# Kernel tuning notes

Measured on AMD Instinct MI355X. Metric: run time of the kernel, lower is better.

## Reference

```python
import jax, jax.numpy as jnp
import numpy as np

B, S, D, E, K = 4, 2048, 1024, 8, 2
H = 4 * D  # SwiGLU hidden size


def setup_inputs() -> dict:
    key = jax.random.key(0)
    ks = jax.random.split(key, 6)
    s = 0.02
    return {
        "x": jax.random.normal(ks[0], (B, S, D), dtype=jnp.float32),
        "Wr": jax.random.normal(ks[1], (D, E), dtype=jnp.float32) * s,
        "br": jnp.zeros((E,), jnp.float32),
        "Wg": jax.random.normal(ks[2], (E, D, H), dtype=jnp.float32) * s,
        "bg": jnp.zeros((E, H), jnp.float32),
        "Wu": jax.random.normal(ks[3], (E, D, H), dtype=jnp.float32) * s,
        "bu": jnp.zeros((E, H), jnp.float32),
        "Wd": jax.random.normal(ks[4], (E, H, D), dtype=jnp.float32) * s,
        "bd": jnp.zeros((E, D), jnp.float32),
        "top_k": K,
    }


def reference(x, Wr, br, Wg, bg, Wu, bu, Wd, bd, top_k):
    # Router: top-k over expert logits, softmax over the selected k values.
    Bx, Sx, Dx = x.shape
    Ex = Wr.shape[-1]
    logits = x @ Wr + br                              # [B,S,E]
    vals, idx = jax.lax.top_k(logits, top_k)          # [B,S,K]
    probs = jax.nn.softmax(vals, axis=-1)             # [B,S,K]
    # Dense per-token expert weight; 0 for experts the token is not routed to.
    gate_w = jnp.sum(jax.nn.one_hot(idx, Ex, dtype=x.dtype) * probs[..., None], axis=-2)  # [B,S,E]

    xt = x.reshape(-1, Dx)          # [T,D]
    gw = gate_w.reshape(-1, Ex).T   # [E,T]

    def body(acc, p):
        wg, bgi, wu, bui, wd, bdi, ge = p
        h = jax.nn.silu(xt @ wg + bgi) * (xt @ wu + bui)   # [T,4D]
        y = (h @ wd + bdi) * ge[:, None]                   # zero where ge==0 (not routed)
        return acc + y, None

    out, _ = jax.lax.scan(body, jnp.zeros_like(xt), (Wg, bg, Wu, bu, Wd, bd, gw))
    return out.reshape(Bx, Sx, Dx)
```

## Files before the change

kernel.cpp:

```cpp
#include <hip/hip_runtime.h>
#include <hip/hip_fp16.h>


#define T_TOK 8192
#define D_IN  1024
#define E_EXP 8
#define H_HID 4096
#define NSLOT (T_TOK * 2)
#define NSLOT_PAD (NSLOT + 256)
#define KSPLIT 4

typedef _Float16 f16;
typedef __attribute__((ext_vector_type(8))) _Float16 f16x8;
typedef __attribute__((ext_vector_type(4))) _Float16 f16x4;
typedef __attribute__((ext_vector_type(4))) float f32x4;

__device__ __forceinline__ void gload_lds16(const void* g, void* l) {
  __builtin_amdgcn_global_load_lds(
      (const __attribute__((address_space(1))) unsigned int*)g,
      (__attribute__((address_space(3))) unsigned int*)l, 16, 0, 0);
}


__global__ __launch_bounds__(256) void prep_kernel(
    const float* __restrict__ x, const float* __restrict__ Wr,
    const float* __restrict__ br, const float* __restrict__ Wg,
    const float* __restrict__ Wu, const float* __restrict__ Wd,
    int* __restrict__ eidx, float2* __restrict__ pval,
    int* __restrict__ counts, f16* __restrict__ xb,
    f16* __restrict__ wgut, f16* __restrict__ wdt) {
  __shared__ float tile[128][33];
  int g = blockIdx.x;
  if (g < T_TOK / 4) {
    int lane = threadIdx.x & 63, wid = threadIdx.x >> 6;
    int t = g * 4 + wid;
    const float* xr = x + (size_t)t * D_IN;
    float s[8] = {0.f, 0.f, 0.f, 0.f, 0.f, 0.f, 0.f, 0.f};
    int dbase = lane * 16;
#pragma unroll
    for (int i = 0; i < 4; ++i) {
      float4 xv = *(const float4*)(xr + dbase + i * 4);
      f16x4 xo = {(f16)xv.x, (f16)xv.y, (f16)xv.z, (f16)xv.w};
      *(f16x4*)(xb + (size_t)t * D_IN + dbase + i * 4) = xo;
      const float xs[4] = {xv.x, xv.y, xv.z, xv.w};
#pragma unroll
      for (int j = 0; j < 4; ++j) {
        const float* wr = Wr + (size_t)(dbase + i * 4 + j) * E_EXP;
        float4 w0 = *(const float4*)wr;
        float4 w1 = *(const float4*)(wr + 4);
        float xvj = xs[j];
        s[0] += xvj * w0.x; s[1] += xvj * w0.y; s[2] += xvj * w0.z; s[3] += xvj * w0.w;
        s[4] += xvj * w1.x; s[5] += xvj * w1.y; s[6] += xvj * w1.z; s[7] += xvj * w1.w;
      }
    }
#pragma unroll
    for (int off = 32; off; off >>= 1)
#pragma unroll
      for (int e = 0; e < 8; ++e) s[e] += __shfl_xor(s[e], off);
    if (lane == 0) {
      float v[8];
#pragma unroll
      for (int e = 0; e < 8; ++e) v[e] = s[e] + br[e];
      int i0 = 0; float v0 = v[0];
#pragma unroll
      for (int e = 1; e < 8; ++e) if (v[e] > v0) { v0 = v[e]; i0 = e; }
      int i1 = -1; float v1 = -1e30f;
#pragma unroll
      for (int e = 0; e < 8; ++e)
        if (e != i0 && v[e] > v1) { v1 = v[e]; i1 = e; }
      float ed = __expf(v1 - v0);
      float inv = 1.f / (1.f + ed);
      eidx[t] = i0 | (i1 << 8);
      pval[t] = make_float2(inv, ed * inv);
      atomicAdd(&counts[i0], 1);
      atomicAdd(&counts[i1], 1);
    }
    return;
  }
  int i = g - T_TOK / 4;
  int which = i >> 13;
  int j = i & 8191;
  const float* src; f16* dst; int R, C, MAP, cx, cy, e; size_t dstride;
  if (which < 2) {
    cx = j & 127; cy = (j >> 7) & 7; e = j >> 10;
    R = D_IN; C = H_HID; dstride = (size_t)2 * H_HID * D_IN;
    dst = wgut; src = (which == 0) ? Wg : Wu; MAP = which + 1;
  } else {
    cx = j & 31; cy = (j >> 5) & 31; e = j >> 10;
    R = H_HID; C = D_IN; dstride = (size_t)D_IN * H_HID;
    dst = wdt; src = Wd; MAP = 0;
  }
  const float* s = src + (size_t)e * R * C;
  f16* d = dst + (size_t)e * dstride;
  int c0 = cx * 32, r0 = cy * 128;
#pragma unroll
  for (int q4 = 0; q4 < 4; ++q4) {
    int q = q4 * 256 + threadIdx.x;
    int r = q >> 3, c4 = (q & 7) * 4;
    float4 v = *(const float4*)(s + (size_t)(r0 + r) * C + c0 + c4);
    tile[r][c4 + 0] = v.x; tile[r][c4 + 1] = v.y;
    tile[r][c4 + 2] = v.z; tile[r][c4 + 3] = v.w;
  }
  __syncthreads();
#pragma unroll
  for (int w2 = 0; w2 < 2; ++w2) {
    int w = w2 * 256 + threadIdx.x;
    int col = w >> 4, oct = w & 15;
    int c = c0 + col;
    int ro = (MAP == 0) ? c : (((c >> 4) << 5) + ((MAP == 2) ? 16 : 0) + (c & 15));
    f16x8 o;
#pragma unroll
    for (int k = 0; k < 8; ++k) o[k] = (f16)tile[oct * 8 + k][col];
    *(f16x8*)(d + (size_t)ro * R + r0 + oct * 8) = o;
  }
}

__global__ void scan_kernel(const int* __restrict__ counts, int* __restrict__ offsets) {
  if (threadIdx.x == 0) {
    int acc = 0;
#pragma unroll
    for (int e = 0; e < E_EXP; ++e) { offsets[e] = acc; acc += counts[e]; }
    offsets[E_EXP] = acc;
  }
}

__global__ __launch_bounds__(256) void scatter_kernel(
    const int* __restrict__ eidx, const float2* __restrict__ pval,
    const int* __restrict__ offsets, int* __restrict__ cursors,
    int* __restrict__ perm, float* __restrict__ gatew, int2* __restrict__ slotAB) {
  int t = blockIdx.x * 256 + threadIdx.x;
  if (t >= T_TOK) return;
  int ei = eidx[t];
  float2 p = pval[t];
  int e0 = ei & 0xff, e1 = (ei >> 8) & 0xff;
  int s0 = offsets[e0] + atomicAdd(&cursors[e0], 1);
  perm[s0] = t; gatew[s0] = p.x;
  int s1 = offsets[e1] + atomicAdd(&cursors[e1], 1);
  perm[s1] = t; gatew[s1] = p.y;
  slotAB[t] = make_int2(s0, s1);
}


#define BAR __builtin_amdgcn_s_barrier()
#define VMCNT(N) asm volatile("s_waitcnt vmcnt(" #N ")" ::: "memory")

#define STAGE_(B, ISB, H, KT, BASE) do {                                   \
  char* d_ = smem + (B)*32768 + (ISB)*16384 + (H)*8192 + wid*1024;         \
  gload_lds16(BASE[(H)*2+0] + (size_t)(KT)*64, d_);                        \
  gload_lds16(BASE[(H)*2+1] + (size_t)(KT)*64, d_ + 4096);                 \
} while (0)

#define LDA_(B, Q)                                                          \
  _Pragma("unroll")                                                         \
  for (int m_ = 0; m_ < 2; ++m_) {                                          \
    fa[m_][0] = *(const f16x8*)(smem + (B)*32768 + aoff + ((Q)*2+m_)*2048 + offk0); \
    fa[m_][1] = *(const f16x8*)(smem + (B)*32768 + aoff + ((Q)*2+m_)*2048 + offk1); \
  }

#define LDB_(FB, B, RH)                                                     \
  _Pragma("unroll")                                                         \
  for (int n_ = 0; n_ < 2; ++n_) {                                          \
    FB[n_][0] = *(const f16x8*)(smem + (B)*32768 + 16384 + boff + ((RH)*2+n_)*2048 + offk0); \
    FB[n_][1] = *(const f16x8*)(smem + (B)*32768 + 16384 + boff + ((RH)*2+n_)*2048 + offk1); \
  }

#define QUAD_(Q, RH, FB)                                                    \
  __builtin_amdgcn_s_setprio(1);                                            \
  _Pragma("unroll")                                                         \
  for (int m_ = 0; m_ < 2; ++m_)                                            \
    _Pragma("unroll")                                                       \
    for (int n_ = 0; n_ < 2; ++n_) {                                        \
      acc[(Q)*2+m_][(RH)*2+n_] = __builtin_amdgcn_mfma_f32_16x16x32_f16(    \
          fa[m_][0], FB[n_][0], acc[(Q)*2+m_][(RH)*2+n_], 0, 0, 0);         \
      acc[(Q)*2+m_][(RH)*2+n_] = __builtin_amdgcn_mfma_f32_16x16x32_f16(    \
          fa[m_][1], FB[n_][1], acc[(Q)*2+m_][(RH)*2+n_], 0, 0, 0);         \
    }                                                                       \
  __builtin_amdgcn_s_setprio(0);

template<int MODE>
__global__ __launch_bounds__(256, 2) void ffn_8ph_kernel(
    const f16* __restrict__ Asrc, const f16* __restrict__ Bsrc,
    const float* __restrict__ bias0, const float* __restrict__ bias1,
    const int* __restrict__ offsets, const int* __restrict__ perm,
    const float* __restrict__ gatew, f16* __restrict__ dst) {
  constexpr int KD = MODE ? H_HID : D_IN;
  constexpr int BROWS = MODE ? D_IN : 2 * H_HID;
  constexpr int NT = 16;

  __shared__ __align__(16) char smem[65536];

  int g = blockIdx.x;
  int xcd = g & 7;
  int e, nt, kc, mt;
  if constexpr (MODE == 0) {
    mt = (g >> 3) & 63;
    int panel = xcd + 8 * (g >> 9);
    e = panel >> 6; nt = panel & 63; kc = 0;
  } else {
    int j = g >> 3;
    nt = j & 7;
    mt = (j >> 3) & 63;
    int group = xcd + 8 * (j >> 9);
    e = group >> 2; kc = group & 3;
  }

  int off = offsets[e];
  int cnt = offsets[e + 1] - off;
  if (mt * 128 >= cnt) return;

  int tid = threadIdx.x, lane = tid & 63, wid = tid >> 6;
  int wm = wid >> 1, wn = wid & 1;
  int l15 = lane & 15, lc0 = lane >> 4, s7 = l15 & 7;
  int aoff = (wm * 64 + l15) * 128;
  int boff = (wn * 64 + l15) * 128;
  int offk0 = ((lc0) ^ s7) * 16;
  int offk1 = ((lc0 + 4) ^ s7) * 16;

  int rowh_[2], lc_[2];
#pragma unroll
  for (int i = 0; i < 2; ++i) {
    int chunk = i * 256 + tid;
    rowh_[i] = chunk >> 3;
    lc_[i] = (chunk & 7) ^ (rowh_[i] & 7);
  }

  const f16 *aB[4], *bB[4];
#pragma unroll
  for (int h = 0; h < 2; ++h)
#pragma unroll
    for (int i = 0; i < 2; ++i) {
      int absrow = h * 64 + rowh_[i];
      bB[h * 2 + i] = Bsrc + ((size_t)e * BROWS + nt * 128 + absrow) * KD +
                      kc * 1024 + lc_[i] * 8;
      int slot = off + min(mt * 128 + absrow, cnt - 1);
      if constexpr (MODE == 0)
        aB[h * 2 + i] = Asrc + (size_t)perm[slot] * KD + lc_[i] * 8;
      else
        aB[h * 2 + i] = Asrc + (size_t)slot * KD + kc * 1024 + lc_[i] * 8;
    }

  float bv0[4], bv1[2];
  if constexpr (MODE == 0) {
#pragma unroll
    for (int p = 0; p < 2; ++p) {
      int h = nt * 64 + wn * 32 + p * 16 + l15;
      bv0[p] = bias0[e * H_HID + h];
      bv1[p] = bias1[e * H_HID + h];
    }
  } else {
#pragma unroll
    for (int n = 0; n < 4; ++n)
      bv0[n] = (kc == 0)
                   ? bias0[e * D_IN + nt * 128 + wn * 64 + n * 16 + l15]
                   : 0.f;
  }

  f32x4 acc[4][4] = {};
  f16x8 fa[2][2], fb01[2][2], fb23[2][2];

  STAGE_(0, 1, 0, 0, bB); STAGE_(0, 1, 1, 0, bB);
  STAGE_(0, 0, 0, 0, aB); STAGE_(0, 0, 1, 0, aB);
  STAGE_(1, 1, 0, 1, bB); STAGE_(1, 1, 1, 1, bB);
  STAGE_(1, 0, 0, 1, aB);
  VMCNT(6);
  BAR;

  for (int it = 0; it < NT / 2; ++it) {
    int b_ = 2 * it + 1;
    int a2 = min(2 * it + 2, NT - 1);
    int b2 = min(2 * it + 3, NT - 1);
    LDA_(0, 0); LDB_(fb01, 0, 0); STAGE_(1, 0, 1, b_, aB);
    BAR; QUAD_(0, 0, fb01); BAR;
    LDB_(fb23, 0, 1);
    BAR; QUAD_(0, 1, fb23); BAR;
    LDA_(0, 1); STAGE_(0, 1, 0, a2, bB);
    BAR; QUAD_(1, 0, fb01); BAR;
    STAGE_(0, 1, 1, a2, bB);
    BAR; QUAD_(1, 1, fb23);
    VMCNT(4);
    BAR;
    LDA_(1, 0); LDB_(fb01, 1, 0); STAGE_(0, 0, 0, a2, aB);
    BAR; QUAD_(0, 0, fb01); BAR;
    LDB_(fb23, 1, 1); STAGE_(0, 0, 1, a2, aB);
    BAR; QUAD_(0, 1, fb23); BAR;
    LDA_(1, 1); STAGE_(1, 1, 0, b2, bB);
    BAR; QUAD_(1, 0, fb01); BAR;
    STAGE_(1, 1, 1, b2, bB); STAGE_(1, 0, 0, b2, aB);
    BAR; QUAD_(1, 1, fb23);
    VMCNT(6);
    BAR;
  }

  VMCNT(0);
  __syncthreads();

  int c0_ = lc0 * 4;
  f16* tile = (f16*)smem;
  if constexpr (MODE == 0) {
#pragma unroll
    for (int p = 0; p < 2; ++p) {
      int colL = wn * 32 + p * 16 + l15;
#pragma unroll
      for (int m = 0; m < 4; ++m) {
        int row = wm * 64 + m * 16 + c0_;
#pragma unroll
        for (int r = 0; r < 4; ++r) {
          float gv = acc[m][2 * p][r] + bv0[p];
          float uv = acc[m][2 * p + 1][r] + bv1[p];
          tile[(row + r) * 64 + colL] = (f16)((gv / (1.f + __expf(-gv))) * uv);
        }
      }
    }
    __syncthreads();
    f16* dbase = dst + (size_t)(off + mt * 128) * H_HID + nt * 64;
#pragma unroll
    for (int i = 0; i < 4; ++i) {
      int linear = i * 256 + tid;
      int row = linear >> 3, c8 = linear & 7;
      if (mt * 128 + row < cnt) {
        f16x8 v = *(const f16x8*)&tile[row * 64 + c8 * 8];
        __builtin_nontemporal_store(v, (f16x8*)(dbase + (size_t)row * H_HID + c8 * 8));
      }
    }
  } else {
#pragma unroll
    for (int n = 0; n < 4; ++n) {
      int colL = wn * 64 + n * 16 + l15;
#pragma unroll
      for (int m = 0; m < 4; ++m) {
        int row = wm * 64 + m * 16 + c0_;
#pragma unroll
        for (int r = 0; r < 4; ++r) {
          int slot = off + min(mt * 128 + row + r, cnt - 1);
          tile[(row + r) * 128 + colL] =
              (f16)(gatew[slot] * (acc[m][n][r] + bv0[n]));
        }
      }
    }
    __syncthreads();
    f16* dstP = dst + (size_t)kc * NSLOT_PAD * D_IN;
    f16* dbase = dstP + (size_t)(off + mt * 128) * D_IN + nt * 128;
#pragma unroll
    for (int i = 0; i < 8; ++i) {
      int linear = i * 256 + tid;
      int row = linear >> 4, c16 = linear & 15;
      if (mt * 128 + row < cnt) {
        f16x8 v = *(const f16x8*)&tile[row * 128 + c16 * 8];
        __builtin_nontemporal_store(v, (f16x8*)(dbase + (size_t)row * D_IN + c16 * 8));
      }
    }
  }
}

__global__ __launch_bounds__(256) void combine_kernel(
    const f16* __restrict__ ypart, const int2* __restrict__ slotAB,
    float* __restrict__ out) {
  int i = blockIdx.x * 256 + threadIdx.x;
  int t = i >> 7;
  int c8 = i & 127;
  int2 s = slotAB[t];
  float sum[8] = {0.f, 0.f, 0.f, 0.f, 0.f, 0.f, 0.f, 0.f};
#pragma unroll
  for (int kc = 0; kc < KSPLIT; ++kc) {
    const f16* base = ypart + (size_t)kc * NSLOT_PAD * D_IN + c8 * 8;
    f16x8 y0 = *(const f16x8*)(base + (size_t)s.x * D_IN);
    f16x8 y1 = *(const f16x8*)(base + (size_t)s.y * D_IN);
#pragma unroll
    for (int j = 0; j < 8; ++j) sum[j] += (float)y0[j] + (float)y1[j];
  }
  float* o = out + (size_t)t * D_IN + c8 * 8;
  f32x4 o0 = {sum[0], sum[1], sum[2], sum[3]};
  f32x4 o1 = {sum[4], sum[5], sum[6], sum[7]};
  __builtin_nontemporal_store(o0, (f32x4*)o);
  __builtin_nontemporal_store(o1, (f32x4*)(o + 4));
}


extern "C" void kernel_launch(void* const* d_in, const int* in_sizes, int n_in,
                              void* d_out, int out_size, void* d_ws, size_t ws_size,
                              hipStream_t stream) {
  const float* x  = (const float*)d_in[0];
  const float* Wr = (const float*)d_in[1];
  const float* br = (const float*)d_in[2];
  const float* Wg = (const float*)d_in[3];
  const float* bg = (const float*)d_in[4];
  const float* Wu = (const float*)d_in[5];
  const float* bu = (const float*)d_in[6];
  const float* Wd = (const float*)d_in[7];
  const float* bd = (const float*)d_in[8];
  float* out = (float*)d_out;

  char* ws = (char*)d_ws;
  size_t o = 0;
  auto alloc = [&](size_t bytes) {
    size_t r = o;
    o += (bytes + 255) & ~(size_t)255;
    return r;
  };
  f16* xb     = (f16*)(ws + alloc((size_t)T_TOK * D_IN * 2));
  f16* wgut   = (f16*)(ws + alloc((size_t)E_EXP * 2 * H_HID * D_IN * 2));
  f16* wdt    = (f16*)(ws + alloc((size_t)E_EXP * D_IN * H_HID * 2));
  f16* hbuf   = (f16*)(ws + alloc((size_t)NSLOT_PAD * H_HID * 2));
  int* eidx   = (int*)(ws + alloc((size_t)T_TOK * 4));
  float2* pval= (float2*)(ws + alloc((size_t)T_TOK * 8));
  int* counts = (int*)(ws + alloc(64 * 4));
  int* cursors = counts + 8;
  int* offsets = counts + 16;
  int* perm   = (int*)(ws + alloc((size_t)NSLOT_PAD * 4));
  float* gatew= (float*)(ws + alloc((size_t)NSLOT_PAD * 4));
  int2* slotAB= (int2*)(ws + alloc((size_t)T_TOK * 8));
  f16* ypart  = xb;

  hipMemsetAsync(counts, 0, 64 * 4, stream);

  prep_kernel<<<dim3(T_TOK / 4 + 3 * 8192), 256, 0, stream>>>(
      x, Wr, br, Wg, Wu, Wd, eidx, pval, counts, xb, wgut, wdt);
  scan_kernel<<<1, 64, 0, stream>>>(counts, offsets);
  scatter_kernel<<<T_TOK / 256, 256, 0, stream>>>(eidx, pval, offsets, cursors,
                                                  perm, gatew, slotAB);
  ffn_8ph_kernel<0><<<dim3(32768), 256, 0, stream>>>(
      xb, wgut, bg, bu, offsets, perm, nullptr, hbuf);
  ffn_8ph_kernel<1><<<dim3(16384), 256, 0, stream>>>(
      hbuf, wdt, bd, nullptr, offsets, nullptr, gatew, ypart);
  combine_kernel<<<T_TOK * D_IN / 8 / 256, 256, 0, stream>>>(ypart, slotAB, out);
}
```

Baseline: 906.3 us.

## Remove split-K from down-projection GEMM and simplify combine to two-slot sum

The down-projection kernel no longer splits the 4096-long reduction into four chunks that each write fp16 partial outputs. Each block now runs the full K loop (64 iterations) and writes one output buffer, with the expert taken directly from the XCD index. The combine kernel then reads only two slot rows per token instead of eight. This removes the write and re-read of the extra partial buffers, at the cost of about four times fewer, longer blocks, less parallelism and per-XCD load imbalance when experts receive uneven token counts.

New measurement: 889.2 us. Within noise of the previous version (-1.9%).

```diff
diff --git a/kernel.cpp b/kernel.cpp
--- a/kernel.cpp
+++ b/kernel.cpp
@@ -8,7 +8,6 @@
 #define H_HID 4096
 #define NSLOT (T_TOK * 2)
 #define NSLOT_PAD (NSLOT + 256)
-#define KSPLIT 4
 
 typedef _Float16 f16;
 typedef __attribute__((ext_vector_type(8))) _Float16 f16x8;
@@ -185,23 +184,22 @@
     const float* __restrict__ gatew, f16* __restrict__ dst) {
   constexpr int KD = MODE ? H_HID : D_IN;
   constexpr int BROWS = MODE ? D_IN : 2 * H_HID;
-  constexpr int NT = 16;
+  constexpr int NT = MODE ? 64 : 16;
 
   __shared__ __align__(16) char smem[65536];
 
   int g = blockIdx.x;
   int xcd = g & 7;
-  int e, nt, kc, mt;
+  int e, nt, mt;
   if constexpr (MODE == 0) {
     mt = (g >> 3) & 63;
     int panel = xcd + 8 * (g >> 9);
-    e = panel >> 6; nt = panel & 63; kc = 0;
+    e = panel >> 6; nt = panel & 63;
   } else {
+    e = xcd;
     int j = g >> 3;
     nt = j & 7;
-    mt = (j >> 3) & 63;
-    int group = xcd + 8 * (j >> 9);
-    e = group >> 2; kc = group & 3;
+    mt = j >> 3;
   }
 
   int off = offsets[e];
@@ -231,12 +229,12 @@
     for (int i = 0; i < 2; ++i) {
       int absrow = h * 64 + rowh_[i];
       bB[h * 2 + i] = Bsrc + ((size_t)e * BROWS + nt * 128 + absrow) * KD +
-                      kc * 1024 + lc_[i] * 8;
+                      lc_[i] * 8;
       int slot = off + min(mt * 128 + absrow, cnt - 1);
       if constexpr (MODE == 0)
         aB[h * 2 + i] = Asrc + (size_t)perm[slot] * KD + lc_[i] * 8;
       else
-        aB[h * 2 + i] = Asrc + (size_t)slot * KD + kc * 1024 + lc_[i] * 8;
+        aB[h * 2 + i] = Asrc + (size_t)slot * KD + lc_[i] * 8;
     }
 
   float bv0[4], bv1[2];
@@ -250,9 +248,7 @@
   } else {
 #pragma unroll
     for (int n = 0; n < 4; ++n)
-      bv0[n] = (kc == 0)
-                   ? bias0[e * D_IN + nt * 128 + wn * 64 + n * 16 + l15]
-                   : 0.f;
+      bv0[n] = bias0[e * D_IN + nt * 128 + wn * 64 + n * 16 + l15];
   }
 
   f32x4 acc[4][4] = {};
@@ -338,8 +334,7 @@
       }
     }
     __syncthreads();
-    f16* dstP = dst + (size_t)kc * NSLOT_PAD * D_IN;
-    f16* dbase = dstP + (size_t)(off + mt * 128) * D_IN + nt * 128;
+    f16* dbase = dst + (size_t)(off + mt * 128) * D_IN + nt * 128;
 #pragma unroll
     for (int i = 0; i < 8; ++i) {
       int linear = i * 256 + tid;
@@ -353,24 +348,19 @@
 }
 
 __global__ __launch_bounds__(256) void combine_kernel(
-    const f16* __restrict__ ypart, const int2* __restrict__ slotAB,
+    const f16* __restrict__ ybuf, const int2* __restrict__ slotAB,
     float* __restrict__ out) {
   int i = blockIdx.x * 256 + threadIdx.x;
   int t = i >> 7;
   int c8 = i & 127;
   int2 s = slotAB[t];
-  float sum[8] = {0.f, 0.f, 0.f, 0.f, 0.f, 0.f, 0.f, 0.f};
-#pragma unroll
-  for (int kc = 0; kc < KSPLIT; ++kc) {
-    const f16* base = ypart + (size_t)kc * NSLOT_PAD * D_IN + c8 * 8;
-    f16x8 y0 = *(const f16x8*)(base + (size_t)s.x * D_IN);
-    f16x8 y1 = *(const f16x8*)(base + (size_t)s.y * D_IN);
-#pragma unroll
-    for (int j = 0; j < 8; ++j) sum[j] += (float)y0[j] + (float)y1[j];
-  }
+  f16x8 y0 = *(const f16x8*)(ybuf + (size_t)s.x * D_IN + c8 * 8);
+  f16x8 y1 = *(const f16x8*)(ybuf + (size_t)s.y * D_IN + c8 * 8);
   float* o = out + (size_t)t * D_IN + c8 * 8;
-  f32x4 o0 = {sum[0], sum[1], sum[2], sum[3]};
-  f32x4 o1 = {sum[4], sum[5], sum[6], sum[7]};
+  f32x4 o0 = {(float)y0[0] + (float)y1[0], (float)y0[1] + (float)y1[1],
+              (float)y0[2] + (float)y1[2], (float)y0[3] + (float)y1[3]};
+  f32x4 o1 = {(float)y0[4] + (float)y1[4], (float)y0[5] + (float)y1[5],
+              (float)y0[6] + (float)y1[6], (float)y0[7] + (float)y1[7]};
   __builtin_nontemporal_store(o0, (f32x4*)o);
   __builtin_nontemporal_store(o1, (f32x4*)(o + 4));
 }
@@ -409,7 +399,7 @@
   int* perm   = (int*)(ws + alloc((size_t)NSLOT_PAD * 4));
   float* gatew= (float*)(ws + alloc((size_t)NSLOT_PAD * 4));
   int2* slotAB= (int2*)(ws + alloc((size_t)T_TOK * 8));
-  f16* ypart  = xb;
+  f16* ybuf   = xb;
 
   hipMemsetAsync(counts, 0, 64 * 4, stream);
 
@@ -420,7 +410,7 @@
                                                   perm, gatew, slotAB);
   ffn_8ph_kernel<0><<<dim3(32768), 256, 0, stream>>>(
       xb, wgut, bg, bu, offsets, perm, nullptr, hbuf);
-  ffn_8ph_kernel<1><<<dim3(16384), 256, 0, stream>>>(
-      hbuf, wdt, bd, nullptr, offsets, nullptr, gatew, ypart);
-  combine_kernel<<<T_TOK * D_IN / 8 / 256, 256, 0, stream>>>(ypart, slotAB, out);
-}
+  ffn_8ph_kernel<1><<<dim3(4096), 256, 0, stream>>>(
+      hbuf, wdt, bd, nullptr, offsets, nullptr, gatew, ybuf);
+  combine_kernel<<<T_TOK * D_IN / 8 / 256, 256, 0, stream>>>(ybuf, slotAB, out);
+}
```
